# Kernel optimization log

Hardware: AMD Instinct MI355X
Metric: run time of the kernel (lower is better)

## Reference

```python
import jax, jax.numpy as jnp
import numpy as np

BETA = 5.0
B, D, K, E2 = 64, 3072, 512, 64


def setup_inputs() -> dict:
    key = jax.random.key(0)
    k1, k2, k3, k4 = jax.random.split(key, 4)
    images = jax.random.normal(k1, (B, D), dtype=jnp.float32)
    w_proj = jax.random.normal(k2, (K, D), dtype=jnp.float32) * 0.02   # project.weight
    w_img2 = jax.random.normal(k3, (K, D * E2), dtype=jnp.float32) * 0.02  # img2.weight
    w_rec = jax.random.normal(k4, (E2, K), dtype=jnp.float32) * 0.02   # rec.weight
    return {"images": images, "w_proj": w_proj, "w_img2": w_img2, "w_rec": w_rec}


def reference(images, w_proj, w_img2, w_rec):
    beta = BETA
    wimg = w_proj.T            # (D, K)
    wrec = w_rec.T             # (K, E2)
    # img2.weight (K, D*E2) -> codebook tensor (K, D, E2), std-normalized over D (ddof=1 to match torch)
    wimg2 = w_img2.reshape(K, D, E2)
    wimg2 = wimg2 / (0.01 + jnp.std(wimg2, axis=1, keepdims=True, ddof=1))

    # ---- encode ----
    xd = images[:, :, None] - wimg[None]          # (B, D, K)
    xh = -jnp.mean(xd * xd, axis=1) * beta        # (B, K)
    xp = jax.nn.softmax(xh, axis=-1)              # (B, K)
    lat1 = xp @ wrec                              # (B, E2)
    xe = jnp.einsum('bdk,kde->bke', xd, wimg2)    # (B, K, E2)
    lat2 = jnp.einsum('bke,bk->be', xe, xp)       # (B, E2)

    # ---- decode ----
    diff = lat1[:, :, None] - wrec.T[None]        # (B, E2, K); wrec.T is (E2, K)
    xh2 = -jnp.mean(diff * diff, axis=1) * beta   # (B, K)
    xp2 = jax.nn.softmax(xh2, axis=-1)            # (B, K)
    xx = xp2[:, :, None] * lat2[:, None, :]       # (B, K, E2)
    xd2 = jnp.einsum('bke,kde->bd', xx, wimg2)    # (B, D)
    images_recon = xp2 @ wimg.T + xd2             # (B, D)

    loss = jnp.mean((images_recon - images) ** 2, axis=-1)  # (B,)
    return loss
```

## Files before the change

kernel.cpp:

```cpp
#include <hip/hip_runtime.h>
#include <math.h>

#define Bn 64
#define Dn 3072
#define Kn 512
#define En 64

static constexpr float BETA = 5.0f;

static constexpr size_t XE_OFF    = 0;
static constexpr size_t S_OFF     = 2097152;
static constexpr size_t DOT_OFF   = 2129920;
static constexpr size_t NPROJ_OFF = 2162688;
static constexpr size_t XP_OFF    = 2163200;
static constexpr size_t LAT1_OFF  = 2195968;
static constexpr size_t LAT2_OFF  = 2200064;
static constexpr size_t XP2_OFF   = 2204160;
static constexpr size_t WRECT_OFF = 2236928;
static constexpr size_t RECON_OFF = 2269696;

typedef float  f4  __attribute__((ext_vector_type(4)));
typedef __bf16 bf8 __attribute__((ext_vector_type(8)));
typedef int    i4  __attribute__((ext_vector_type(4)));

union AB { i4 i; bf8 b; };

__device__ __forceinline__ unsigned short bf16b(float x) {
  __bf16 h = (__bf16)x;
  union Cv { __bf16 h; unsigned short u; } c;
  c.h = h;
  return c.u;
}

__device__ __forceinline__ float waveAllMax(float v) {
#pragma unroll
  for (int o = 32; o; o >>= 1) v = fmaxf(v, __shfl_xor(v, o));
  return v;
}
__device__ __forceinline__ float waveAllSum(float v) {
#pragma unroll
  for (int o = 32; o; o >>= 1) v += __shfl_xor(v, o);
  return v;
}

__global__ __launch_bounds__(256) void kPrep(const float* __restrict__ img,
                                             float* __restrict__ ws) {
  const int t = threadIdx.x, ds = blockIdx.x;
  const int T = t >> 6, l = t & 63;
  const int b = 16 * T + (l & 15);
  const int d0 = 32 * ds + 8 * (l >> 4);
  const float* p = img + (size_t)b * Dn + d0;
  unsigned short u[8];
#pragma unroll
  for (int j = 0; j < 8; ++j) u[j] = bf16b(p[j]);
  i4 v;
  v.x = (int)u[0] | ((int)u[1] << 16);
  v.y = (int)u[2] | ((int)u[3] << 16);
  v.z = (int)u[4] | ((int)u[5] << 16);
  v.w = (int)u[6] | ((int)u[7] << 16);
  ((i4*)(ws + RECON_OFF))[(ds * 4 + T) * 64 + l] = v;
}

__global__ __launch_bounds__(256) void kTr(const float* __restrict__ wrec, float* __restrict__ ws) {
  int g = blockIdx.x * 256 + threadIdx.x;
  int k = g >> 6, e = g & 63;
  ws[WRECT_OFF + g] = wrec[(size_t)e * Kn + k];
}

__global__ __launch_bounds__(256) void kDot(const float* __restrict__ wproj,
                                            float* __restrict__ ws) {
  const int t = threadIdx.x, w = t >> 6, l = t & 63, elane = l & 15, dgrp = l >> 4;
  const int kk = blockIdx.x * 16 + elane;
  const unsigned short* afr16 = (const unsigned short*)(ws + RECON_OFF);
  const i4* afr = (const i4*)afr16;
  const float* wrow = wproj + (size_t)kk * Dn;
  f4 acc = {0.f, 0.f, 0.f, 0.f};
  float np = 0.f;
  float bwA[8], bwB[8];
  i4 avA, avB;
  avA = afr[(0 * 4 + w) * 64 + l];
#pragma unroll
  for (int j = 0; j < 8; ++j) bwA[j] = wrow[8 * dgrp + j];

#define KD_ITER(BWC, BWN, AVC, AVN, N) {                                         \
    const int np1 = (N) + 1;                                                     \
    if (np1 < 96) {                                                              \
      AVN = afr[(np1 * 4 + w) * 64 + l];                                         \
      _Pragma("unroll")                                                          \
      for (int j = 0; j < 8; ++j) BWN[j] = wrow[(size_t)np1 * 32 + 8 * dgrp + j];\
    }                                                                            \
    bf8 bfr;                                                                     \
    _Pragma("unroll")                                                            \
    for (int j = 0; j < 8; ++j) { float v = BWC[j]; np = fmaf(v, v, np); bfr[j] = (__bf16)v; } \
    AB a; a.i = AVC;                                                             \
    acc = __builtin_amdgcn_mfma_f32_16x16x32_bf16(a.b, bfr, acc, 0, 0, 0);       \
  }

  for (int n = 0; n < 96; n += 2) {
    KD_ITER(bwA, bwB, avA, avB, n)
    KD_ITER(bwB, bwA, avB, avA, n + 1)
  }
#undef KD_ITER
#pragma unroll
  for (int r = 0; r < 4; ++r) {
    int b = 16 * w + 4 * dgrp + r;
    ws[DOT_OFF + (size_t)b * Kn + kk] = acc[r];
  }
  np += __shfl_xor(np, 16);
  np += __shfl_xor(np, 32);
  if (w == 0 && dgrp == 0) ws[NPROJ_OFF + kk] = np;
}

__global__ __launch_bounds__(256) void kA(const float* __restrict__ wproj,
                                          const float* __restrict__ w2,
                                          float* __restrict__ ws) {
  const int k = blockIdx.x, t = threadIdx.x;
  const int w = t >> 6, l = t & 63, elane = l & 15, dgrp = l >> 4;
  const int ecol = 16 * w + elane;
  __shared__ float wp[Dn];
  __shared__ i4 bufA0[256], bufA1[256];
  const float* wpk = wproj + (size_t)k * Dn;
#pragma unroll
  for (int i = 0; i < 3; ++i) ((f4*)wp)[t + 256 * i] = ((const f4*)wpk)[t + 256 * i];
  const i4* afr = (const i4*)(ws + RECON_OFF);
  const float* w2k = w2 + (size_t)k * (Dn * En);
  f4 acc0 = {0.f,0.f,0.f,0.f}, acc1 = {0.f,0.f,0.f,0.f};
  f4 acc2 = {0.f,0.f,0.f,0.f}, acc3 = {0.f,0.f,0.f,0.f};
  float ssum = 0.f, ssq = 0.f, pacc = 0.f;
  float bwA[8], bwB[8];
  i4 avP = afr[(0 * 4 + w) * 64 + l];
#pragma unroll
  for (int j = 0; j < 8; ++j) bwA[j] = w2k[(size_t)(8 * dgrp + j) * 64 + ecol];
  bufA0[w * 64 + l] = avP;
  __syncthreads();

#define KA_ITER(BWC, BWN, BUFC, BUFN, N) {                                       \
    const int np1 = (N) + 1; i4 avn;                                             \
    if (np1 < 96) {                                                              \
      avn = afr[(np1 * 4 + w) * 64 + l];                                         \
      _Pragma("unroll")                                                          \
      for (int j = 0; j < 8; ++j)                                                \
        BWN[j] = w2k[(size_t)(np1 * 32 + 8 * dgrp + j) * 64 + ecol];             \
    }                                                                            \
    bf8 bfr;                                                                     \
    _Pragma("unroll")                                                            \
    for (int j = 0; j < 8; ++j) {                                                \
      float v = BWC[j];                                                          \
      ssum += v; ssq = fmaf(v, v, ssq);                                          \
      pacc = fmaf(wp[(N) * 32 + 8 * dgrp + j], v, pacc);                         \
      bfr[j] = (__bf16)v;                                                        \
    }                                                                            \
    AB a0, a1, a2, a3;                                                           \
    a0.i = BUFC[0 * 64 + l]; a1.i = BUFC[1 * 64 + l];                            \
    a2.i = BUFC[2 * 64 + l]; a3.i = BUFC[3 * 64 + l];                            \
    acc0 = __builtin_amdgcn_mfma_f32_16x16x32_bf16(a0.b, bfr, acc0, 0, 0, 0);    \
    acc1 = __builtin_amdgcn_mfma_f32_16x16x32_bf16(a1.b, bfr, acc1, 0, 0, 0);    \
    acc2 = __builtin_amdgcn_mfma_f32_16x16x32_bf16(a2.b, bfr, acc2, 0, 0, 0);    \
    acc3 = __builtin_amdgcn_mfma_f32_16x16x32_bf16(a3.b, bfr, acc3, 0, 0, 0);    \
    if (np1 < 96) BUFN[w * 64 + l] = avn;                                        \
    __syncthreads();                                                             \
  }

  for (int n = 0; n < 96; n += 2) {
    KA_ITER(bwA, bwB, bufA0, bufA1, n)
    KA_ITER(bwB, bwA, bufA1, bufA0, n + 1)
  }
#undef KA_ITER

  ssum += __shfl_xor(ssum, 16); ssum += __shfl_xor(ssum, 32);
  ssq  += __shfl_xor(ssq, 16);  ssq  += __shfl_xor(ssq, 32);
  pacc += __shfl_xor(pacc, 16); pacc += __shfl_xor(pacc, 32);
  float var = (ssq - ssum * ssum * (1.0f / Dn)) * (1.0f / (Dn - 1));
  float sv = 1.0f / (0.01f + sqrtf(fmaxf(var, 0.f)));
  if (dgrp == 0) ws[S_OFF + (size_t)k * En + ecol] = sv;
#pragma unroll
  for (int T = 0; T < 4; ++T) {
    f4 a = (T == 0) ? acc0 : (T == 1) ? acc1 : (T == 2) ? acc2 : acc3;
#pragma unroll
    for (int r = 0; r < 4; ++r) {
      int b = 16 * T + 4 * dgrp + r;
      ws[XE_OFF + ((size_t)b * Kn + k) * En + ecol] = sv * (a[r] - pacc);
    }
  }
}

__global__ __launch_bounds__(256) void kMid1(const float* __restrict__ img,
                                             float* __restrict__ ws) {
  const int b = blockIdx.x;
  const int t = threadIdx.x;
  const int wid = t >> 6, lane = t & 63;
  __shared__ float xp_sh[512];
  __shared__ float red[16];
  __shared__ float scratch[256];

  float acc = 0.f;
  const f4* irow = (const f4*)(img + (size_t)b * Dn);
#pragma unroll
  for (int i = 0; i < 3; ++i) {
    f4 v = irow[t + 256 * i];
    acc = fmaf(v.x, v.x, acc); acc = fmaf(v.y, v.y, acc);
    acc = fmaf(v.z, v.z, acc); acc = fmaf(v.w, v.w, acc);
  }
  acc = waveAllSum(acc);
  if (lane == 0) red[wid] = acc;
  __syncthreads();
  const float nimg = red[0] + red[1] + red[2] + red[3];

  const float c = -(BETA / Dn);
  float d1 = ws[DOT_OFF + (size_t)b * Kn + t];
  float d2 = ws[DOT_OFF + (size_t)b * Kn + t + 256];
  float np1 = ws[NPROJ_OFF + t];
  float np2 = ws[NPROJ_OFF + t + 256];
  float x1 = c * (nimg - 2.f * d1 + np1);
  float x2 = c * (nimg - 2.f * d2 + np2);

  float m = waveAllMax(fmaxf(x1, x2));
  if (lane == 0) red[4 + wid] = m;
  __syncthreads();
  m = fmaxf(fmaxf(red[4], red[5]), fmaxf(red[6], red[7]));
  float e1 = expf(x1 - m), e2 = expf(x2 - m);
  float sv = waveAllSum(e1 + e2);
  if (lane == 0) red[8 + wid] = sv;
  __syncthreads();
  float inv = 1.f / (red[8] + red[9] + red[10] + red[11]);
  float p1 = e1 * inv, p2 = e2 * inv;
  xp_sh[t] = p1; xp_sh[t + 256] = p2;
  ws[XP_OFF + (size_t)b * Kn + t] = p1;
  ws[XP_OFF + (size_t)b * Kn + t + 256] = p2;
  __syncthreads();

  const int e = t & 63, q = t >> 6;
  float lacc = 0.f;
  for (int kk = q * 128; kk < q * 128 + 128; ++kk)
    lacc = fmaf(xp_sh[kk], ws[WRECT_OFF + (size_t)kk * En + e], lacc);
  scratch[q * 64 + e] = lacc;
  __syncthreads();
  if (t < 64)
    ws[LAT1_OFF + (size_t)b * En + t] =
        scratch[t] + scratch[64 + t] + scratch[128 + t] + scratch[192 + t];
}

__global__ __launch_bounds__(256) void kMid2(float* __restrict__ ws) {
  const int b = blockIdx.x;
  const int t = threadIdx.x;
  const int wid = t >> 6, lane = t & 63;
  __shared__ float xp_sh[512];
  __shared__ __align__(16) float l1_sh[64];
  __shared__ float scratch[256];
  __shared__ float red[16];

  xp_sh[t] = ws[XP_OFF + (size_t)b * Kn + t];
  xp_sh[t + 256] = ws[XP_OFF + (size_t)b * Kn + t + 256];
  if (t < 64) l1_sh[t] = ws[LAT1_OFF + (size_t)b * En + t];
  __syncthreads();

  const int e = t & 63, q = t >> 6;
  const float* xeb = ws + XE_OFF + (size_t)b * Kn * En;
  float lacc = 0.f;
  for (int kk = q * 128; kk < q * 128 + 128; ++kk)
    lacc = fmaf(xp_sh[kk], xeb[(size_t)kk * En + e], lacc);
  scratch[q * 64 + e] = lacc;
  __syncthreads();
  if (t < 64)
    ws[LAT2_OFF + (size_t)b * En + t] =
        scratch[t] + scratch[64 + t] + scratch[128 + t] + scratch[192 + t];

  float h1 = 0.f, h2 = 0.f;
#pragma unroll
  for (int i = 0; i < 16; ++i) {
    f4 lv = *(const f4*)&l1_sh[i * 4];
    f4 w1 = *(const f4*)&ws[WRECT_OFF + (size_t)t * En + i * 4];
    f4 w2v = *(const f4*)&ws[WRECT_OFF + ((size_t)t + 256) * En + i * 4];
    float a0 = lv.x - w1.x, a1 = lv.y - w1.y, a2 = lv.z - w1.z, a3 = lv.w - w1.w;
    h1 = fmaf(a0, a0, h1); h1 = fmaf(a1, a1, h1);
    h1 = fmaf(a2, a2, h1); h1 = fmaf(a3, a3, h1);
    float b0 = lv.x - w2v.x, b1 = lv.y - w2v.y, b2 = lv.z - w2v.z, b3 = lv.w - w2v.w;
    h2 = fmaf(b0, b0, h2); h2 = fmaf(b1, b1, h2);
    h2 = fmaf(b2, b2, h2); h2 = fmaf(b3, b3, h2);
  }
  const float c2 = -(BETA / En);
  float x1 = c2 * h1, x2 = c2 * h2;

  float m = waveAllMax(fmaxf(x1, x2));
  if (lane == 0) red[4 + wid] = m;
  __syncthreads();
  m = fmaxf(fmaxf(red[4], red[5]), fmaxf(red[6], red[7]));
  float e1 = expf(x1 - m), e2 = expf(x2 - m);
  float sv = waveAllSum(e1 + e2);
  if (lane == 0) red[8 + wid] = sv;
  __syncthreads();
  float inv = 1.f / (red[8] + red[9] + red[10] + red[11]);
  float p1 = e1 * inv, p2 = e2 * inv;
  ws[XP2_OFF + (size_t)b * Kn + t] = p1;
  ws[XP2_OFF + (size_t)b * Kn + t + 256] = p2;
  unsigned short* xpb = (unsigned short*)(ws + DOT_OFF);
  xpb[(size_t)b * Kn + t] = bf16b(p1);
  xpb[(size_t)b * Kn + t + 256] = bf16b(p2);
}

__global__ __launch_bounds__(256) void kZ(float* __restrict__ ws) {
  const int g = blockIdx.x * 256 + threadIdx.x;
  const int S = g >> 8;
  const int T = (g >> 6) & 3;
  const int l = g & 63;
  const int dgrp = l >> 4;
  const int b = 16 * T + (l & 15);
  const int kd0 = S * 32 + 8 * dgrp;
  const int k = kd0 >> 6;
  const int e0 = kd0 & 63;
  const float xp2v = ws[XP2_OFF + (size_t)b * Kn + k];
  unsigned short u[8];
#pragma unroll
  for (int j = 0; j < 8; ++j) {
    float v = xp2v * ws[LAT2_OFF + (size_t)b * En + e0 + j] * ws[S_OFF + (size_t)k * En + e0 + j];
    u[j] = bf16b(v);
  }
  i4 v;
  v.x = (int)u[0] | ((int)u[1] << 16);
  v.y = (int)u[2] | ((int)u[3] << 16);
  v.z = (int)u[4] | ((int)u[5] << 16);
  v.w = (int)u[6] | ((int)u[7] << 16);
  ((i4*)(ws + XE_OFF))[g] = v;
}

__global__ __launch_bounds__(256) void kRecon(const float* __restrict__ wproj,
                                              float* __restrict__ ws) {
  const int blk = blockIdx.x, t = threadIdx.x;
  const int w = t >> 6, l = t & 63, elane = l & 15, dgrp = l >> 4;
  const int dA = blk * 64 + 16 * w + elane;
  const unsigned short* xpb = (const unsigned short*)(ws + DOT_OFF);
  f4 acc0 = {0.f,0.f,0.f,0.f}, acc1 = {0.f,0.f,0.f,0.f};
  f4 acc2 = {0.f,0.f,0.f,0.f}, acc3 = {0.f,0.f,0.f,0.f};
  for (int n = 0; n < 16; ++n) {
    bf8 afr;
#pragma unroll
    for (int j = 0; j < 8; ++j)
      afr[j] = (__bf16)wproj[(size_t)(32 * n + 8 * dgrp + j) * Dn + dA];
    AB b0, b1, b2, b3;
    b0.i = *(const i4*)&xpb[(size_t)(0 * 16 + elane) * Kn + 32 * n + 8 * dgrp];
    b1.i = *(const i4*)&xpb[(size_t)(1 * 16 + elane) * Kn + 32 * n + 8 * dgrp];
    b2.i = *(const i4*)&xpb[(size_t)(2 * 16 + elane) * Kn + 32 * n + 8 * dgrp];
    b3.i = *(const i4*)&xpb[(size_t)(3 * 16 + elane) * Kn + 32 * n + 8 * dgrp];
    acc0 = __builtin_amdgcn_mfma_f32_16x16x32_bf16(afr, b0.b, acc0, 0, 0, 0);
    acc1 = __builtin_amdgcn_mfma_f32_16x16x32_bf16(afr, b1.b, acc1, 0, 0, 0);
    acc2 = __builtin_amdgcn_mfma_f32_16x16x32_bf16(afr, b2.b, acc2, 0, 0, 0);
    acc3 = __builtin_amdgcn_mfma_f32_16x16x32_bf16(afr, b3.b, acc3, 0, 0, 0);
  }
#pragma unroll
  for (int T = 0; T < 4; ++T) {
    f4 a = (T == 0) ? acc0 : (T == 1) ? acc1 : (T == 2) ? acc2 : acc3;
#pragma unroll
    for (int r = 0; r < 4; ++r) {
      int bb = 16 * T + elane;
      int dd = blk * 64 + 16 * w + 4 * dgrp + r;
      ws[RECON_OFF + (size_t)bb * Dn + dd] = a[r];
    }
  }
}

__global__ __launch_bounds__(256) void kB(const float* __restrict__ w2,
                                          float* __restrict__ ws) {
  const int dtile = blockIdx.x, ks = blockIdx.y, t = threadIdx.x;
  const int w = t >> 6, l = t & 63, elane = l & 15, dgrp = l >> 4;
  const int d = dtile * 64 + 16 * w + elane;
  __shared__ i4 bufZ0[256], bufZ1[256];
  const i4* zfr = (const i4*)(ws + XE_OFF);
  f4 acc0 = {0.f,0.f,0.f,0.f}, acc1 = {0.f,0.f,0.f,0.f};
  f4 acc2 = {0.f,0.f,0.f,0.f}, acc3 = {0.f,0.f,0.f,0.f};
  float bwA[8], bwB[8];
  i4 avP = zfr[((ks * 64 + 0) * 4 + w) * 64 + l];
  {
    const int kk = ks * 32;
    const float* p = w2 + ((size_t)kk * Dn + d) * En + 8 * dgrp;
#pragma unroll
    for (int j = 0; j < 8; ++j) bwA[j] = p[j];
  }
  bufZ0[w * 64 + l] = avP;
  __syncthreads();

#define KB_ITER(BWC, BWN, BUFC, BUFN, N) {                                       \
    const int np1 = (N) + 1; i4 avn;                                             \
    if (np1 < 64) {                                                              \
      avn = zfr[((ks * 64 + np1) * 4 + w) * 64 + l];                             \
      const int kk = ks * 32 + (np1 >> 1);                                       \
      const int e0 = (np1 & 1) * 32;                                             \
      const float* p = w2 + ((size_t)kk * Dn + d) * En + e0 + 8 * dgrp;          \
      _Pragma("unroll")                                                          \
      for (int j = 0; j < 8; ++j) BWN[j] = p[j];                                 \
    }                                                                            \
    bf8 bfr;                                                                     \
    _Pragma("unroll")                                                            \
    for (int j = 0; j < 8; ++j) bfr[j] = (__bf16)BWC[j];                         \
    AB a0, a1, a2, a3;                                                           \
    a0.i = BUFC[0 * 64 + l]; a1.i = BUFC[1 * 64 + l];                            \
    a2.i = BUFC[2 * 64 + l]; a3.i = BUFC[3 * 64 + l];                            \
    acc0 = __builtin_amdgcn_mfma_f32_16x16x32_bf16(a0.b, bfr, acc0, 0, 0, 0);    \
    acc1 = __builtin_amdgcn_mfma_f32_16x16x32_bf16(a1.b, bfr, acc1, 0, 0, 0);    \
    acc2 = __builtin_amdgcn_mfma_f32_16x16x32_bf16(a2.b, bfr, acc2, 0, 0, 0);    \
    acc3 = __builtin_amdgcn_mfma_f32_16x16x32_bf16(a3.b, bfr, acc3, 0, 0, 0);    \
    if (np1 < 64) BUFN[w * 64 + l] = avn;                                        \
    __syncthreads();                                                             \
  }

  for (int n = 0; n < 64; n += 2) {
    KB_ITER(bwA, bwB, bufZ0, bufZ1, n)
    KB_ITER(bwB, bwA, bufZ1, bufZ0, n + 1)
  }
#undef KB_ITER

#pragma unroll
  for (int T = 0; T < 4; ++T) {
    f4 a = (T == 0) ? acc0 : (T == 1) ? acc1 : (T == 2) ? acc2 : acc3;
#pragma unroll
    for (int r = 0; r < 4; ++r) {
      int b = 16 * T + 4 * dgrp + r;
      atomicAdd(&ws[RECON_OFF + (size_t)b * Dn + d], a[r]);
    }
  }
}

__global__ __launch_bounds__(256) void kLoss(const float* __restrict__ img,
                                             const float* __restrict__ ws,
                                             float* __restrict__ out) {
  const int b = blockIdx.x, t = threadIdx.x;
  __shared__ float red[4];
  float acc = 0.f;
  const f4* r4 = (const f4*)(ws + RECON_OFF + (size_t)b * Dn);
  const f4* i4p = (const f4*)(img + (size_t)b * Dn);
#pragma unroll
  for (int i = 0; i < 3; ++i) {
    f4 r = r4[t + 256 * i], v = i4p[t + 256 * i];
    float dx = r.x - v.x, dy = r.y - v.y, dz = r.z - v.z, dw = r.w - v.w;
    acc = fmaf(dx, dx, acc); acc = fmaf(dy, dy, acc);
    acc = fmaf(dz, dz, acc); acc = fmaf(dw, dw, acc);
  }
  acc = waveAllSum(acc);
  if ((t & 63) == 0) red[t >> 6] = acc;
  __syncthreads();
  if (t == 0) out[b] = (red[0] + red[1] + red[2] + red[3]) * (1.0f / Dn);
}

extern "C" void kernel_launch(void* const* d_in, const int* in_sizes, int n_in,
                              void* d_out, int out_size, void* d_ws, size_t ws_size,
                              hipStream_t stream) {
  const float* img   = (const float*)d_in[0];
  const float* wproj = (const float*)d_in[1];
  const float* w2    = (const float*)d_in[2];
  const float* wrec  = (const float*)d_in[3];
  float* ws  = (float*)d_ws;
  float* out = (float*)d_out;

  hipLaunchKernelGGL(kPrep,  dim3(96),  dim3(256), 0, stream, img, ws);
  hipLaunchKernelGGL(kTr,    dim3(128), dim3(256), 0, stream, wrec, ws);
  hipLaunchKernelGGL(kDot,   dim3(32),  dim3(256), 0, stream, wproj, ws);
  hipLaunchKernelGGL(kA,     dim3(512), dim3(256), 0, stream, wproj, w2, ws);
  hipLaunchKernelGGL(kMid1,  dim3(64),  dim3(256), 0, stream, img, ws);
  hipLaunchKernelGGL(kMid2,  dim3(64),  dim3(256), 0, stream, ws);
  hipLaunchKernelGGL(kZ,     dim3(1024),dim3(256), 0, stream, ws);
  hipLaunchKernelGGL(kRecon, dim3(48),  dim3(256), 0, stream, wproj, ws);
  hipLaunchKernelGGL(kB,     dim3(48, 16), dim3(256), 0, stream, w2, ws);
  hipLaunchKernelGGL(kLoss,  dim3(64),  dim3(256), 0, stream, img, ws, out);
}
```

Baseline: 245.0 us.

## Fuse recon GEMM into kB, replace atomics with partials, drop LDS staging

Removes the kRecon kernel by folding the xp2 @ w_proj term into kB, where each k-slice block adds one extra MFMA step. kB now writes per-slice partial sums instead of using atomicAdd, and kLoss reduces the 16 partials. kA and kB stop staging A fragments through shared memory with a barrier every step and instead load all four fragments per lane straight into registers. This cuts a kernel launch, the atomics and the barriers, but adds redundant global fragment loads and a larger partial buffer that kLoss must read.

```diff
diff --git a/kernel.cpp b/kernel.cpp
--- a/kernel.cpp
+++ b/kernel.cpp
@@ -17,7 +17,8 @@
 static constexpr size_t LAT2_OFF  = 2200064;
 static constexpr size_t XP2_OFF   = 2204160;
 static constexpr size_t WRECT_OFF = 2236928;
-static constexpr size_t RECON_OFF = 2269696;
+static constexpr size_t FRAG_OFF  = 2269696;
+static constexpr size_t PART_OFF  = 2269696;
 
 typedef float  f4  __attribute__((ext_vector_type(4)));
 typedef __bf16 bf8 __attribute__((ext_vector_type(8)));
@@ -58,7 +59,7 @@
   v.y = (int)u[2] | ((int)u[3] << 16);
   v.z = (int)u[4] | ((int)u[5] << 16);
   v.w = (int)u[6] | ((int)u[7] << 16);
-  ((i4*)(ws + RECON_OFF))[(ds * 4 + T) * 64 + l] = v;
+  ((i4*)(ws + FRAG_OFF))[(ds * 4 + T) * 64 + l] = v;
 }
 
 __global__ __launch_bounds__(256) void kTr(const float* __restrict__ wrec, float* __restrict__ ws) {
@@ -71,8 +72,7 @@
                                             float* __restrict__ ws) {
   const int t = threadIdx.x, w = t >> 6, l = t & 63, elane = l & 15, dgrp = l >> 4;
   const int kk = blockIdx.x * 16 + elane;
-  const unsigned short* afr16 = (const unsigned short*)(ws + RECON_OFF);
-  const i4* afr = (const i4*)afr16;
+  const i4* afr = (const i4*)(ws + FRAG_OFF);
   const float* wrow = wproj + (size_t)kk * Dn;
   f4 acc = {0.f, 0.f, 0.f, 0.f};
   float np = 0.f;
@@ -118,29 +118,31 @@
   const int w = t >> 6, l = t & 63, elane = l & 15, dgrp = l >> 4;
   const int ecol = 16 * w + elane;
   __shared__ float wp[Dn];
-  __shared__ i4 bufA0[256], bufA1[256];
   const float* wpk = wproj + (size_t)k * Dn;
 #pragma unroll
   for (int i = 0; i < 3; ++i) ((f4*)wp)[t + 256 * i] = ((const f4*)wpk)[t + 256 * i];
-  const i4* afr = (const i4*)(ws + RECON_OFF);
+  __syncthreads();
+
+  const i4* afr = (const i4*)(ws + FRAG_OFF);
   const float* w2k = w2 + (size_t)k * (Dn * En);
   f4 acc0 = {0.f,0.f,0.f,0.f}, acc1 = {0.f,0.f,0.f,0.f};
   f4 acc2 = {0.f,0.f,0.f,0.f}, acc3 = {0.f,0.f,0.f,0.f};
   float ssum = 0.f, ssq = 0.f, pacc = 0.f;
   float bwA[8], bwB[8];
-  i4 avP = afr[(0 * 4 + w) * 64 + l];
+  i4 avA[4], avB[4];
 #pragma unroll
   for (int j = 0; j < 8; ++j) bwA[j] = w2k[(size_t)(8 * dgrp + j) * 64 + ecol];
-  bufA0[w * 64 + l] = avP;
-  __syncthreads();
-
-#define KA_ITER(BWC, BWN, BUFC, BUFN, N) {                                       \
-    const int np1 = (N) + 1; i4 avn;                                             \
+#pragma unroll
+  for (int T = 0; T < 4; ++T) avA[T] = afr[T * 64 + l];
+
+#define KA_ITER(BWC, BWN, AVC, AVN, N) {                                         \
+    const int np1 = (N) + 1;                                                     \
     if (np1 < 96) {                                                              \
-      avn = afr[(np1 * 4 + w) * 64 + l];                                         \
       _Pragma("unroll")                                                          \
       for (int j = 0; j < 8; ++j)                                                \
         BWN[j] = w2k[(size_t)(np1 * 32 + 8 * dgrp + j) * 64 + ecol];             \
+      _Pragma("unroll")                                                          \
+      for (int T = 0; T < 4; ++T) AVN[T] = afr[(np1 * 4 + T) * 64 + l];          \
     }                                                                            \
     bf8 bfr;                                                                     \
     _Pragma("unroll")                                                            \
@@ -151,19 +153,16 @@
       bfr[j] = (__bf16)v;                                                        \
     }                                                                            \
     AB a0, a1, a2, a3;                                                           \
-    a0.i = BUFC[0 * 64 + l]; a1.i = BUFC[1 * 64 + l];                            \
-    a2.i = BUFC[2 * 64 + l]; a3.i = BUFC[3 * 64 + l];                            \
+    a0.i = AVC[0]; a1.i = AVC[1]; a2.i = AVC[2]; a3.i = AVC[3];                  \
     acc0 = __builtin_amdgcn_mfma_f32_16x16x32_bf16(a0.b, bfr, acc0, 0, 0, 0);    \
     acc1 = __builtin_amdgcn_mfma_f32_16x16x32_bf16(a1.b, bfr, acc1, 0, 0, 0);    \
     acc2 = __builtin_amdgcn_mfma_f32_16x16x32_bf16(a2.b, bfr, acc2, 0, 0, 0);    \
     acc3 = __builtin_amdgcn_mfma_f32_16x16x32_bf16(a3.b, bfr, acc3, 0, 0, 0);    \
-    if (np1 < 96) BUFN[w * 64 + l] = avn;                                        \
-    __syncthreads();                                                             \
   }
 
   for (int n = 0; n < 96; n += 2) {
-    KA_ITER(bwA, bwB, bufA0, bufA1, n)
-    KA_ITER(bwB, bwA, bufA1, bufA0, n + 1)
+    KA_ITER(bwA, bwB, avA, avB, n)
+    KA_ITER(bwB, bwA, avB, avA, n + 1)
   }
 #undef KA_ITER
 
@@ -323,90 +322,71 @@
   ((i4*)(ws + XE_OFF))[g] = v;
 }
 
-__global__ __launch_bounds__(256) void kRecon(const float* __restrict__ wproj,
-                                              float* __restrict__ ws) {
-  const int blk = blockIdx.x, t = threadIdx.x;
-  const int w = t >> 6, l = t & 63, elane = l & 15, dgrp = l >> 4;
-  const int dA = blk * 64 + 16 * w + elane;
-  const unsigned short* xpb = (const unsigned short*)(ws + DOT_OFF);
-  f4 acc0 = {0.f,0.f,0.f,0.f}, acc1 = {0.f,0.f,0.f,0.f};
-  f4 acc2 = {0.f,0.f,0.f,0.f}, acc3 = {0.f,0.f,0.f,0.f};
-  for (int n = 0; n < 16; ++n) {
-    bf8 afr;
-#pragma unroll
-    for (int j = 0; j < 8; ++j)
-      afr[j] = (__bf16)wproj[(size_t)(32 * n + 8 * dgrp + j) * Dn + dA];
-    AB b0, b1, b2, b3;
-    b0.i = *(const i4*)&xpb[(size_t)(0 * 16 + elane) * Kn + 32 * n + 8 * dgrp];
-    b1.i = *(const i4*)&xpb[(size_t)(1 * 16 + elane) * Kn + 32 * n + 8 * dgrp];
-    b2.i = *(const i4*)&xpb[(size_t)(2 * 16 + elane) * Kn + 32 * n + 8 * dgrp];
-    b3.i = *(const i4*)&xpb[(size_t)(3 * 16 + elane) * Kn + 32 * n + 8 * dgrp];
-    acc0 = __builtin_amdgcn_mfma_f32_16x16x32_bf16(afr, b0.b, acc0, 0, 0, 0);
-    acc1 = __builtin_amdgcn_mfma_f32_16x16x32_bf16(afr, b1.b, acc1, 0, 0, 0);
-    acc2 = __builtin_amdgcn_mfma_f32_16x16x32_bf16(afr, b2.b, acc2, 0, 0, 0);
-    acc3 = __builtin_amdgcn_mfma_f32_16x16x32_bf16(afr, b3.b, acc3, 0, 0, 0);
-  }
-#pragma unroll
-  for (int T = 0; T < 4; ++T) {
-    f4 a = (T == 0) ? acc0 : (T == 1) ? acc1 : (T == 2) ? acc2 : acc3;
-#pragma unroll
-    for (int r = 0; r < 4; ++r) {
-      int bb = 16 * T + elane;
-      int dd = blk * 64 + 16 * w + 4 * dgrp + r;
-      ws[RECON_OFF + (size_t)bb * Dn + dd] = a[r];
-    }
-  }
-}
-
-__global__ __launch_bounds__(256) void kB(const float* __restrict__ w2,
+__global__ __launch_bounds__(256) void kB(const float* __restrict__ wproj,
+                                          const float* __restrict__ w2,
                                           float* __restrict__ ws) {
   const int dtile = blockIdx.x, ks = blockIdx.y, t = threadIdx.x;
   const int w = t >> 6, l = t & 63, elane = l & 15, dgrp = l >> 4;
   const int d = dtile * 64 + 16 * w + elane;
-  __shared__ i4 bufZ0[256], bufZ1[256];
   const i4* zfr = (const i4*)(ws + XE_OFF);
   f4 acc0 = {0.f,0.f,0.f,0.f}, acc1 = {0.f,0.f,0.f,0.f};
   f4 acc2 = {0.f,0.f,0.f,0.f}, acc3 = {0.f,0.f,0.f,0.f};
-  float bwA[8], bwB[8];
-  i4 avP = zfr[((ks * 64 + 0) * 4 + w) * 64 + l];
+  f4 bwA[2], bwB[2];
+  i4 avA[4], avB[4];
   {
-    const int kk = ks * 32;
-    const float* p = w2 + ((size_t)kk * Dn + d) * En + 8 * dgrp;
-#pragma unroll
-    for (int j = 0; j < 8; ++j) bwA[j] = p[j];
-  }
-  bufZ0[w * 64 + l] = avP;
-  __syncthreads();
-
-#define KB_ITER(BWC, BWN, BUFC, BUFN, N) {                                       \
-    const int np1 = (N) + 1; i4 avn;                                             \
+    const f4* p = (const f4*)(w2 + ((size_t)(ks * 32) * Dn + d) * En + 8 * dgrp);
+    bwA[0] = p[0]; bwA[1] = p[1];
+#pragma unroll
+    for (int T = 0; T < 4; ++T) avA[T] = zfr[((ks * 64) * 4 + T) * 64 + l];
+  }
+
+#define KB_ITER(BWC, BWN, AVC, AVN, N) {                                         \
+    const int np1 = (N) + 1;                                                     \
     if (np1 < 64) {                                                              \
-      avn = zfr[((ks * 64 + np1) * 4 + w) * 64 + l];                             \
       const int kk = ks * 32 + (np1 >> 1);                                       \
       const int e0 = (np1 & 1) * 32;                                             \
-      const float* p = w2 + ((size_t)kk * Dn + d) * En + e0 + 8 * dgrp;          \
+      const f4* p = (const f4*)(w2 + ((size_t)kk * Dn + d) * En + e0 + 8 * dgrp);\
+      BWN[0] = p[0]; BWN[1] = p[1];                                              \
       _Pragma("unroll")                                                          \
-      for (int j = 0; j < 8; ++j) BWN[j] = p[j];                                 \
+      for (int T = 0; T < 4; ++T) AVN[T] = zfr[((ks * 64 + np1) * 4 + T) * 64 + l]; \
     }                                                                            \
     bf8 bfr;                                                                     \
     _Pragma("unroll")                                                            \
-    for (int j = 0; j < 8; ++j) bfr[j] = (__bf16)BWC[j];                         \
+    for (int j = 0; j < 4; ++j) {                                                \
+      bfr[j] = (__bf16)BWC[0][j];                                                \
+      bfr[4 + j] = (__bf16)BWC[1][j];                                            \
+    }                                                                            \
     AB a0, a1, a2, a3;                                                           \
-    a0.i = BUFC[0 * 64 + l]; a1.i = BUFC[1 * 64 + l];                            \
-    a2.i = BUFC[2 * 64 + l]; a3.i = BUFC[3 * 64 + l];                            \
+    a0.i = AVC[0]; a1.i = AVC[1]; a2.i = AVC[2]; a3.i = AVC[3];                  \
     acc0 = __builtin_amdgcn_mfma_f32_16x16x32_bf16(a0.b, bfr, acc0, 0, 0, 0);    \
     acc1 = __builtin_amdgcn_mfma_f32_16x16x32_bf16(a1.b, bfr, acc1, 0, 0, 0);    \
     acc2 = __builtin_amdgcn_mfma_f32_16x16x32_bf16(a2.b, bfr, acc2, 0, 0, 0);    \
     acc3 = __builtin_amdgcn_mfma_f32_16x16x32_bf16(a3.b, bfr, acc3, 0, 0, 0);    \
-    if (np1 < 64) BUFN[w * 64 + l] = avn;                                        \
-    __syncthreads();                                                             \
   }
 
   for (int n = 0; n < 64; n += 2) {
-    KB_ITER(bwA, bwB, bufZ0, bufZ1, n)
-    KB_ITER(bwB, bwA, bufZ1, bufZ0, n + 1)
+    KB_ITER(bwA, bwB, avA, avB, n)
+    KB_ITER(bwB, bwA, avB, avA, n + 1)
   }
 #undef KB_ITER
+
+  {
+    const int kk0 = ks * 32;
+    bf8 bw;
+#pragma unroll
+    for (int j = 0; j < 8; ++j)
+      bw[j] = (__bf16)wproj[(size_t)(kk0 + 8 * dgrp + j) * Dn + d];
+    const unsigned short* xpb = (const unsigned short*)(ws + DOT_OFF);
+    AB a0, a1, a2, a3;
+    a0.i = *(const i4*)&xpb[(size_t)(0 * 16 + elane) * Kn + kk0 + 8 * dgrp];
+    a1.i = *(const i4*)&xpb[(size_t)(1 * 16 + elane) * Kn + kk0 + 8 * dgrp];
+    a2.i = *(const i4*)&xpb[(size_t)(2 * 16 + elane) * Kn + kk0 + 8 * dgrp];
+    a3.i = *(const i4*)&xpb[(size_t)(3 * 16 + elane) * Kn + kk0 + 8 * dgrp];
+    acc0 = __builtin_amdgcn_mfma_f32_16x16x32_bf16(a0.b, bw, acc0, 0, 0, 0);
+    acc1 = __builtin_amdgcn_mfma_f32_16x16x32_bf16(a1.b, bw, acc1, 0, 0, 0);
+    acc2 = __builtin_amdgcn_mfma_f32_16x16x32_bf16(a2.b, bw, acc2, 0, 0, 0);
+    acc3 = __builtin_amdgcn_mfma_f32_16x16x32_bf16(a3.b, bw, acc3, 0, 0, 0);
+  }
 
 #pragma unroll
   for (int T = 0; T < 4; ++T) {
@@ -414,7 +394,7 @@
 #pragma unroll
     for (int r = 0; r < 4; ++r) {
       int b = 16 * T + 4 * dgrp + r;
-      atomicAdd(&ws[RECON_OFF + (size_t)b * Dn + d], a[r]);
+      ws[PART_OFF + ((size_t)ks * Bn + b) * Dn + d] = a[r];
     }
   }
 }
@@ -425,11 +405,17 @@
   const int b = blockIdx.x, t = threadIdx.x;
   __shared__ float red[4];
   float acc = 0.f;
-  const f4* r4 = (const f4*)(ws + RECON_OFF + (size_t)b * Dn);
+  const f4* p4 = (const f4*)(ws + PART_OFF);
   const f4* i4p = (const f4*)(img + (size_t)b * Dn);
+  const int rowq = Dn / 4;
 #pragma unroll
   for (int i = 0; i < 3; ++i) {
-    f4 r = r4[t + 256 * i], v = i4p[t + 256 * i];
+    int idx = t + 256 * i;
+    f4 r = {0.f, 0.f, 0.f, 0.f};
+#pragma unroll
+    for (int s = 0; s < 16; ++s)
+      r += p4[((size_t)s * Bn + b) * rowq + idx];
+    f4 v = i4p[idx];
     float dx = r.x - v.x, dy = r.y - v.y, dz = r.z - v.z, dw = r.w - v.w;
     acc = fmaf(dx, dx, acc); acc = fmaf(dy, dy, acc);
     acc = fmaf(dz, dz, acc); acc = fmaf(dw, dw, acc);
@@ -457,7 +443,6 @@
   hipLaunchKernelGGL(kMid1,  dim3(64),  dim3(256), 0, stream, img, ws);
   hipLaunchKernelGGL(kMid2,  dim3(64),  dim3(256), 0, stream, ws);
   hipLaunchKernelGGL(kZ,     dim3(1024),dim3(256), 0, stream, ws);
-  hipLaunchKernelGGL(kRecon, dim3(48),  dim3(256), 0, stream, wproj, ws);
-  hipLaunchKernelGGL(kB,     dim3(48, 16), dim3(256), 0, stream, w2, ws);
+  hipLaunchKernelGGL(kB,     dim3(48, 16), dim3(256), 0, stream, wproj, w2, ws);
   hipLaunchKernelGGL(kLoss,  dim3(64),  dim3(256), 0, stream, img, ws, out);
 }
```

Measured after the change: 262.2 us. +7.0%, slower.
